# Performance work log

Hardware: AMD Instinct MI355X
Metric: run time of the kernel (lower is better)

## Reference

```python
import jax, jax.numpy as jnp
import numpy as np

EMBED_DIM = 1024
NUM_HEADS = 16
HEAD_DIM = EMBED_DIM // NUM_HEADS


def setup_inputs() -> dict:
    key = jax.random.key(0)
    ks = jax.random.split(key, 9)
    B, S, D = 2, 2048, EMBED_DIM
    scale = 1.0 / np.sqrt(D)
    x = jax.random.normal(ks[0], (B, S, D), dtype=jnp.float32)
    wq = jax.random.normal(ks[1], (D, D), dtype=jnp.float32) * scale
    bq = jax.random.normal(ks[2], (D,), dtype=jnp.float32) * 0.02
    wk = jax.random.normal(ks[3], (D, D), dtype=jnp.float32) * scale
    bk = jax.random.normal(ks[4], (D,), dtype=jnp.float32) * 0.02
    wv = jax.random.normal(ks[5], (D, D), dtype=jnp.float32) * scale
    bv = jax.random.normal(ks[6], (D,), dtype=jnp.float32) * 0.02
    wo = jax.random.normal(ks[7], (D, D), dtype=jnp.float32) * scale
    bo = jax.random.normal(ks[8], (D,), dtype=jnp.float32) * 0.02
    return {"x": x, "wq": wq, "bq": bq, "wk": wk, "bk": bk,
            "wv": wv, "bv": bv, "wo": wo, "bo": bo}


def reference(x, wq, bq, wk, bk, wv, bv, wo, bo):
    B, S, D = x.shape
    H, Hd = NUM_HEADS, HEAD_DIM
    # separate QKV linears (weights stored [in, out] so x @ w)
    q = (x @ wq + bq).reshape(B, S, H, Hd).transpose(0, 2, 1, 3)  # [B,H,S,Hd]
    k = (x @ wk + bk).reshape(B, S, H, Hd).transpose(0, 2, 1, 3)
    v = (x @ wv + bv).reshape(B, S, H, Hd).transpose(0, 2, 1, 3)
    scores = jnp.einsum('bhqd,bhkd->bhqk', q, k) / jnp.sqrt(jnp.float32(Hd))
    attn = jax.nn.softmax(scores, axis=-1)
    context = jnp.einsum('bhqk,bhkd->bhqd', attn, v)
    context = context.transpose(0, 2, 1, 3).reshape(B, S, D)
    return context @ wo + bo
```

## Files before the change

### kernel.cpp

```cpp
#include <hip/hip_runtime.h>
#include <cstdint>
#include <cstddef>


typedef float floatx4 __attribute__((ext_vector_type(4)));
typedef __bf16 bf16x8 __attribute__((ext_vector_type(8)));
union ABFrag { bf16x8 v; uint4 q; unsigned short u[8]; unsigned int w[4]; };

__device__ __forceinline__ unsigned short f2bf(float f) {
    unsigned int u = __builtin_bit_cast(unsigned int, f);
    return (unsigned short)((u + 0x7FFFu + ((u >> 16) & 1u)) >> 16);
}

__device__ __forceinline__ unsigned int pkbf(float lo, float hi) {
    unsigned int a = __builtin_bit_cast(unsigned int, hi) + 0x8000u;
    unsigned int b = __builtin_bit_cast(unsigned int, lo) + 0x8000u;
    return __builtin_amdgcn_perm(a, b, 0x07060302u);
}

#if __has_builtin(__builtin_amdgcn_exp2f)
#define EXP2F(x) __builtin_amdgcn_exp2f(x)
#else
#define EXP2F(x) exp2f(x)
#endif

__device__ __forceinline__ void glds16(const void* g, void* l) {
    __builtin_amdgcn_global_load_lds(
        (const __attribute__((address_space(1))) unsigned int*)(uintptr_t)g,
        (__attribute__((address_space(3))) unsigned int*)(unsigned int)(uintptr_t)l,
        16, 0, 0);
}

__global__ void convert_x_kernel(const float* __restrict__ x,
                                 unsigned short* __restrict__ xb) {
    int i = (blockIdx.x * 256 + threadIdx.x) * 8;
    float4 a = *(const float4*)(x + i);
    float4 b = *(const float4*)(x + i + 4);
    union { unsigned short u[8]; uint4 q; } o;
    o.u[0] = f2bf(a.x); o.u[1] = f2bf(a.y); o.u[2] = f2bf(a.z); o.u[3] = f2bf(a.w);
    o.u[4] = f2bf(b.x); o.u[5] = f2bf(b.y); o.u[6] = f2bf(b.z); o.u[7] = f2bf(b.w);
    *(uint4*)(xb + i) = o.q;
}

__global__ void convert_wT_kernel(const float* __restrict__ w0, const float* __restrict__ w1,
                                  const float* __restrict__ w2, const float* __restrict__ w3,
                                  unsigned short* __restrict__ wT) {
    __shared__ unsigned short t[32][40];
    const float* w = (blockIdx.z == 0) ? w0 : (blockIdx.z == 1) ? w1
                   : (blockIdx.z == 2) ? w2 : w3;
    unsigned short* dst = wT + (size_t)blockIdx.z * 1024 * 1024;
    const int k0 = blockIdx.x * 32, n0 = blockIdx.y * 32;
    const int tid = threadIdx.x;
    {
        int ry = tid >> 3, cx = (tid & 7) * 4;
        float4 v = *(const float4*)(w + (size_t)(k0 + ry) * 1024 + n0 + cx);
        t[cx + 0][ry] = f2bf(v.x); t[cx + 1][ry] = f2bf(v.y);
        t[cx + 2][ry] = f2bf(v.z); t[cx + 3][ry] = f2bf(v.w);
    }
    __syncthreads();
    int n = tid >> 3, kc = (tid & 7) * 4;
    *(uint2*)(dst + (size_t)(n0 + n) * 1024 + k0 + kc) = *(const uint2*)&t[n][kc];
}

template<int KIND>
__launch_bounds__(256, 2)
__global__ void gemm_kernel(const unsigned short* __restrict__ A,
                            const unsigned short* __restrict__ wT,
                            const float* __restrict__ bias0,
                            const float* __restrict__ bias1,
                            const float* __restrict__ bias2,
                            void* __restrict__ out0,
                            void* __restrict__ out1,
                            void* __restrict__ out2)
{
    __shared__ unsigned short a_s[128 * 32];
    __shared__ unsigned short b_s[128 * 32];

    const int tid  = threadIdx.x;
    const int wid  = tid >> 6;
    const int lane = tid & 63;
    const int quad = lane >> 4;
    const int l15  = lane & 15;
    const int wm   = (wid >> 1) * 64;
    const int wn   = (wid & 1) * 64;
    const int m0   = blockIdx.y * 128;
    const int n0   = blockIdx.x * 128;

    const unsigned short* Bt = (KIND == 0) ? wT + (size_t)blockIdx.z * (1024 * 1024) : wT;
    const float* bias = (KIND == 0)
        ? (blockIdx.z == 0 ? bias0 : blockIdx.z == 1 ? bias1 : bias2) : bias0;

    const int sr = lane >> 2;
    const int sc = (lane & 3) * 8;
    const unsigned short* gA = A  + (size_t)(m0 + wid * 32 + sr) * 1024 + sc;
    const unsigned short* gB = Bt + (size_t)(n0 + wid * 32 + sr) * 1024 + sc;
    unsigned short* lA = a_s + wid * 1024;
    unsigned short* lB = b_s + wid * 1024;

    floatx4 acc[4][4];
    #pragma unroll
    for (int i = 0; i < 4; i++)
        #pragma unroll
        for (int j = 0; j < 4; j++)
            acc[i][j] = floatx4{0.f, 0.f, 0.f, 0.f};

    for (int k0 = 0; k0 < 1024; k0 += 32) {
        __syncthreads();
        glds16(gA + k0,             lA);
        glds16(gA + k0 + 16 * 1024, lA + 512);
        glds16(gB + k0,             lB);
        glds16(gB + k0 + 16 * 1024, lB + 512);
        __syncthreads();

        ABFrag af[4], bf4[4];
        #pragma unroll
        for (int i = 0; i < 4; i++)
            af[i].q = *(const uint4*)(a_s + (wm + i * 16 + l15) * 32 + quad * 8);
        #pragma unroll
        for (int j = 0; j < 4; j++)
            bf4[j].q = *(const uint4*)(b_s + (wn + j * 16 + l15) * 32 + quad * 8);
        #pragma unroll
        for (int i = 0; i < 4; i++)
            #pragma unroll
            for (int j = 0; j < 4; j++)
                acc[i][j] = __builtin_amdgcn_mfma_f32_16x16x32_bf16(
                    af[i].v, bf4[j].v, acc[i][j], 0, 0, 0);
    }

    if constexpr (KIND == 1) {
        float* out = (float*)out0;
        #pragma unroll
        for (int j = 0; j < 4; j++) {
            int gn = n0 + wn + j * 16 + l15;
            float bval = bias[gn];
            #pragma unroll
            for (int i = 0; i < 4; i++)
                #pragma unroll
                for (int r = 0; r < 4; r++) {
                    int gm = m0 + wm + i * 16 + quad * 4 + r;
                    out[(size_t)gm * 1024 + gn] = acc[i][j][r] + bval;
                }
        }
    } else {
        if (blockIdx.z == 0) {
            const float SCQ = 0.125f * 1.44269504088896f;
            unsigned short* out = (unsigned short*)out0;
            #pragma unroll
            for (int j = 0; j < 4; j++) {
                int gn = n0 + wn + j * 16 + l15;
                float bval = bias[gn];
                int h = gn >> 6, d = gn & 63;
                #pragma unroll
                for (int i = 0; i < 4; i++)
                    #pragma unroll
                    for (int r = 0; r < 4; r++) {
                        int gm = m0 + wm + i * 16 + quad * 4 + r;
                        int b = gm >> 11, s = gm & 2047;
                        out[(((size_t)(b * 16 + h) * 2048 + s) << 6) + d] =
                            f2bf((acc[i][j][r] + bval) * SCQ);
                    }
            }
        } else if (blockIdx.z == 1) {
            unsigned short* out = (unsigned short*)out1;
            #pragma unroll
            for (int j = 0; j < 4; j++) {
                int gn = n0 + wn + j * 16 + l15;
                float bval = bias[gn];
                int h = gn >> 6, d = gn & 63;
                int dg = d >> 3, dl = d & 7;
                #pragma unroll
                for (int i = 0; i < 4; i++)
                    #pragma unroll
                    for (int r = 0; r < 4; r++) {
                        int gm = m0 + wm + i * 16 + quad * 4 + r;
                        int b = gm >> 11, s = gm & 2047;
                        int dphys = ((dg ^ (s & 7)) << 3) | dl;
                        out[(((size_t)(b * 16 + h) * 2048 + s) << 6) + dphys] =
                            f2bf(acc[i][j][r] + bval);
                    }
            }
        } else {
            __shared__ unsigned short t_s[128][136];
            #pragma unroll
            for (int j = 0; j < 4; j++) {
                int nl = wn + j * 16 + l15;
                float bval = bias[n0 + nl];
                #pragma unroll
                for (int i = 0; i < 4; i++)
                    #pragma unroll
                    for (int r = 0; r < 4; r++)
                        t_s[nl][wm + i * 16 + quad * 4 + r] = f2bf(acc[i][j][r] + bval);
            }
            __syncthreads();
            unsigned short* out = (unsigned short*)out2;
            const int n  = tid >> 1, half = tid & 1;
            const int bh = (m0 >> 11) * 16 + ((n0 + n) >> 6);
            const int d  = (n0 + n) & 63;
            const int chunk = ((m0 & 2047) >> 6) + half;
            const int dmask = d & 7;
            unsigned short* dstb = out + ((size_t)(bh * 32 + chunk) * 64 + d) * 64;
            const unsigned short* src = &t_s[n][half * 64];
            #pragma unroll
            for (int gp = 0; gp < 8; gp++) {
                int u1 = 32 * (gp >> 2) + 4 * (gp & 3);
                uint2 lo = *(const uint2*)(src + u1);
                uint2 hi = *(const uint2*)(src + u1 + 16);
                unsigned short* dq = dstb + ((gp ^ dmask) << 3);
                *(uint2*)dq       = lo;
                *(uint2*)(dq + 4) = hi;
            }
        }
    }
}

__launch_bounds__(256, 2)
__global__ void attn_kernel(const unsigned short* __restrict__ Q,
                            const unsigned short* __restrict__ K,
                            const unsigned short* __restrict__ Vt,
                            unsigned short* __restrict__ ctx)
{
    __shared__ unsigned short smem[2][2][4096];

    const int tid  = threadIdx.x;
    const int wid  = tid >> 6;
    const int lane = tid & 63;
    const int quad = lane >> 4;
    const int l15  = lane & 15;
    const int xr   = l15 & 7;

    const int bh = blockIdx.y;
    const unsigned short* Qh = Q + (size_t)bh * (2048 * 64);
    const char* Kc = (const char*)(K  + (size_t)bh * (2048 * 64));
    const char* Vc = (const char*)(Vt + (size_t)bh * (2048 * 64));
    const int q0 = blockIdx.x * 128 + wid * 32;

    ABFrag qf[2][2];
    #pragma unroll
    for (int jq = 0; jq < 2; jq++)
        #pragma unroll
        for (int s = 0; s < 2; s++)
            qf[jq][s].q = *(const uint4*)(Qh + (size_t)(q0 + jq * 16 + l15) * 64
                                          + s * 32 + quad * 8);

    int kcol[2], vcol[2];
    kcol[0] = ((quad    ) ^ xr) << 3;
    kcol[1] = ((quad + 4) ^ xr) << 3;
    vcol[0] = ((quad    ) ^ xr) << 3;
    vcol[1] = ((quad + 4) ^ xr) << 3;

    floatx4 acc[4][2];
    #pragma unroll
    for (int i = 0; i < 4; i++)
        #pragma unroll
        for (int jq = 0; jq < 2; jq++)
            acc[i][jq] = floatx4{0.f, 0.f, 0.f, 0.f};
    float lrun[2] = {0.f, 0.f};

    auto stage = [&](int c, int b) {
        const char* gk = Kc + (size_t)c * 8192 + wid * 2048 + lane * 16;
        char* lk = (char*)&smem[b][0][0] + wid * 2048;
        glds16(gk,        lk);
        glds16(gk + 1024, lk + 1024);
        const char* gv = Vc + (size_t)c * 8192 + wid * 2048 + lane * 16;
        char* lv = (char*)&smem[b][1][0] + wid * 2048;
        glds16(gv,        lv);
        glds16(gv + 1024, lv + 1024);
    };

    stage(0, 0);

    for (int c = 0; c < 32; ++c) {
        const int b = c & 1;
        __syncthreads();
        if (c + 1 < 32) stage(c + 1, b ^ 1);

        const unsigned short* ks = &smem[b][0][0];
        const unsigned short* vs = &smem[b][1][0];

        floatx4 st[4][2];
        #pragma unroll
        for (int kt = 0; kt < 4; kt++) {
            ABFrag k0, k1;
            const unsigned short* kr = ks + (kt * 16 + l15) * 64;
            k0.q = *(const uint4*)(kr + kcol[0]);
            k1.q = *(const uint4*)(kr + kcol[1]);
            #pragma unroll
            for (int jq = 0; jq < 2; jq++) {
                floatx4 t = floatx4{0.f, 0.f, 0.f, 0.f};
                t = __builtin_amdgcn_mfma_f32_16x16x32_bf16(k0.v, qf[jq][0].v, t, 0, 0, 0);
                t = __builtin_amdgcn_mfma_f32_16x16x32_bf16(k1.v, qf[jq][1].v, t, 0, 0, 0);
                st[kt][jq] = t;
            }
        }

        unsigned int pk[4][2][2];
        #pragma unroll
        for (int jq = 0; jq < 2; jq++) {
            float ls = 0.f;
            #pragma unroll
            for (int kt = 0; kt < 4; kt++) {
                #pragma unroll
                for (int t2 = 0; t2 < 2; t2++) {
                    float p0 = EXP2F(st[kt][jq][2 * t2 + 0]);
                    float p1 = EXP2F(st[kt][jq][2 * t2 + 1]);
                    ls += p0 + p1;
                    pk[kt][jq][t2] = pkbf(p0, p1);
                }
            }
            lrun[jq] += ls;
        }

        #pragma unroll
        for (int s2 = 0; s2 < 2; s2++) {
            ABFrag pf[2];
            #pragma unroll
            for (int jq = 0; jq < 2; jq++) {
                pf[jq].w[0] = pk[2 * s2 + 0][jq][0];
                pf[jq].w[1] = pk[2 * s2 + 0][jq][1];
                pf[jq].w[2] = pk[2 * s2 + 1][jq][0];
                pf[jq].w[3] = pk[2 * s2 + 1][jq][1];
            }
            #pragma unroll
            for (int i = 0; i < 4; i++) {
                ABFrag vf;
                vf.q = *(const uint4*)(vs + (i * 16 + l15) * 64 + vcol[s2]);
                #pragma unroll
                for (int jq = 0; jq < 2; jq++)
                    acc[i][jq] = __builtin_amdgcn_mfma_f32_16x16x32_bf16(
                        vf.v, pf[jq].v, acc[i][jq], 0, 0, 0);
            }
        }
    }

    const int b_ = bh >> 4, h = bh & 15;
    #pragma unroll
    for (int jq = 0; jq < 2; jq++) {
        float s = lrun[jq];
        s += __shfl_xor(s, 16, 64);
        s += __shfl_xor(s, 32, 64);
        float inv = 1.0f / s;
        int q = q0 + jq * 16 + l15;
        size_t base = (size_t)(b_ * 2048 + q) * 1024 + h * 64;
        #pragma unroll
        for (int i = 0; i < 4; i++) {
            float v0 = acc[i][jq][0] * inv, v1 = acc[i][jq][1] * inv;
            float v2 = acc[i][jq][2] * inv, v3 = acc[i][jq][3] * inv;
            uint2 w2 = make_uint2(pkbf(v0, v1), pkbf(v2, v3));
            *(uint2*)(ctx + base + i * 16 + quad * 4) = w2;
        }
    }
}

extern "C" void kernel_launch(void* const* d_in, const int* in_sizes, int n_in,
                              void* d_out, int out_size, void* d_ws, size_t ws_size,
                              hipStream_t stream)
{
    const float* x  = (const float*)d_in[0];
    const float* wq = (const float*)d_in[1];
    const float* bq = (const float*)d_in[2];
    const float* wk = (const float*)d_in[3];
    const float* bk = (const float*)d_in[4];
    const float* wv = (const float*)d_in[5];
    const float* bv = (const float*)d_in[6];
    const float* wo = (const float*)d_in[7];
    const float* bo = (const float*)d_in[8];

    const size_t NE = (size_t)4096 * 1024;
    unsigned short* xb  = (unsigned short*)d_ws;
    unsigned short* wT  = xb  + NE;
    unsigned short* qb  = wT  + NE;
    unsigned short* kb  = qb  + NE;
    unsigned short* vtb = kb  + NE;
    unsigned short* ctx = vtb + NE;

    hipLaunchKernelGGL(convert_x_kernel, dim3(2048), dim3(256), 0, stream, x, xb);
    hipLaunchKernelGGL(convert_wT_kernel, dim3(32, 32, 4), dim3(256), 0, stream,
                       wq, wk, wv, wo, wT);
    hipLaunchKernelGGL((gemm_kernel<0>), dim3(8, 32, 3), dim3(256), 0, stream,
                       xb, wT, bq, bk, bv, (void*)qb, (void*)kb, (void*)vtb);
    hipLaunchKernelGGL(attn_kernel, dim3(16, 32), dim3(256), 0, stream, qb, kb, vtb, ctx);
    hipLaunchKernelGGL((gemm_kernel<1>), dim3(8, 32), dim3(256), 0, stream,
                       ctx, wT + 3 * NE / 4, bo, nullptr, nullptr, d_out, nullptr, nullptr);
}
```

Measured before the change: 197.3 us.

## Swap MFMA operands for vectorized epilogues and halve attention tile per wave

The QK projection GEMM swaps its MFMA operand order so each lane holds four consecutive output columns, which lets the Q/K and output-projection epilogues write packed uint2 or float4 stores instead of scalar ones. V is split into its own GEMM instantiation that writes the transposed, swizzled layout directly from registers, removing the LDS transpose buffer and its extra barrier. The attention kernel drops to 16 queries per wave (64 per block, twice as many blocks) to cut register use and raise occupancy, at the cost of reloading K/V tiles for twice as many blocks. Launch bounds are raised to allow more resident blocks, and the QKV projection now takes two launches instead of one.

```diff
diff --git a/kernel.cpp b/kernel.cpp
--- a/kernel.cpp
+++ b/kernel.cpp
@@ -63,15 +63,13 @@
 }
 
 template<int KIND>
-__launch_bounds__(256, 2)
+__launch_bounds__(256, 3)
 __global__ void gemm_kernel(const unsigned short* __restrict__ A,
-                            const unsigned short* __restrict__ wT,
+                            const unsigned short* __restrict__ Bt,
                             const float* __restrict__ bias0,
                             const float* __restrict__ bias1,
-                            const float* __restrict__ bias2,
                             void* __restrict__ out0,
-                            void* __restrict__ out1,
-                            void* __restrict__ out2)
+                            void* __restrict__ out1)
 {
     __shared__ unsigned short a_s[128 * 32];
     __shared__ unsigned short b_s[128 * 32];
@@ -86,14 +84,14 @@
     const int m0   = blockIdx.y * 128;
     const int n0   = blockIdx.x * 128;
 
-    const unsigned short* Bt = (KIND == 0) ? wT + (size_t)blockIdx.z * (1024 * 1024) : wT;
-    const float* bias = (KIND == 0)
-        ? (blockIdx.z == 0 ? bias0 : blockIdx.z == 1 ? bias1 : bias2) : bias0;
+    const int z = (KIND == 0) ? blockIdx.z : 0;
+    const unsigned short* Bw = Bt + (size_t)z * (1024 * 1024);
+    const float* bias = (KIND == 0 && z == 1) ? bias1 : bias0;
 
     const int sr = lane >> 2;
     const int sc = (lane & 3) * 8;
     const unsigned short* gA = A  + (size_t)(m0 + wid * 32 + sr) * 1024 + sc;
-    const unsigned short* gB = Bt + (size_t)(n0 + wid * 32 + sr) * 1024 + sc;
+    const unsigned short* gB = Bw + (size_t)(n0 + wid * 32 + sr) * 1024 + sc;
     unsigned short* lA = a_s + wid * 1024;
     unsigned short* lB = b_s + wid * 1024;
 
@@ -122,98 +120,80 @@
         #pragma unroll
         for (int i = 0; i < 4; i++)
             #pragma unroll
-            for (int j = 0; j < 4; j++)
-                acc[i][j] = __builtin_amdgcn_mfma_f32_16x16x32_bf16(
-                    af[i].v, bf4[j].v, acc[i][j], 0, 0, 0);
-    }
-
-    if constexpr (KIND == 1) {
+            for (int j = 0; j < 4; j++) {
+                if (KIND == 1)
+                    acc[i][j] = __builtin_amdgcn_mfma_f32_16x16x32_bf16(
+                        af[i].v, bf4[j].v, acc[i][j], 0, 0, 0);
+                else
+                    acc[i][j] = __builtin_amdgcn_mfma_f32_16x16x32_bf16(
+                        bf4[i].v, af[j].v, acc[i][j], 0, 0, 0);
+            }
+    }
+
+    if constexpr (KIND == 2) {
         float* out = (float*)out0;
+        #pragma unroll
+        for (int i = 0; i < 4; i++) {
+            int gnb = n0 + wn + i * 16 + quad * 4;
+            float4 bv4 = *(const float4*)(bias + gnb);
+            #pragma unroll
+            for (int j = 0; j < 4; j++) {
+                int gm = m0 + wm + j * 16 + l15;
+                float4 o = make_float4(acc[i][j][0] + bv4.x, acc[i][j][1] + bv4.y,
+                                       acc[i][j][2] + bv4.z, acc[i][j][3] + bv4.w);
+                *(float4*)(out + (size_t)gm * 1024 + gnb) = o;
+            }
+        }
+    } else if constexpr (KIND == 0) {
+        const float SCQ = 0.125f * 1.44269504088896f;
+        unsigned short* out = (unsigned short*)(z == 0 ? out0 : out1);
+        #pragma unroll
+        for (int i = 0; i < 4; i++) {
+            int gnb = n0 + wn + i * 16 + quad * 4;
+            float4 bv4 = *(const float4*)(bias + gnb);
+            int h = gnb >> 6, db = gnb & 63;
+            #pragma unroll
+            for (int j = 0; j < 4; j++) {
+                int s = m0 + wm + j * 16 + l15;
+                int b = s >> 11, srow = s & 2047;
+                size_t rowb = ((size_t)(b * 16 + h) * 2048 + srow) * 64;
+                float v0 = acc[i][j][0] + bv4.x, v1 = acc[i][j][1] + bv4.y;
+                float v2 = acc[i][j][2] + bv4.z, v3 = acc[i][j][3] + bv4.w;
+                size_t addr;
+                if (z == 0) {
+                    v0 *= SCQ; v1 *= SCQ; v2 *= SCQ; v3 *= SCQ;
+                    addr = rowb + db;
+                } else {
+                    addr = rowb + (size_t)((((db >> 3) ^ (srow & 7)) << 3) + (db & 7));
+                }
+                uint2 w2 = make_uint2(pkbf(v0, v1), pkbf(v2, v3));
+                *(uint2*)(out + addr) = w2;
+            }
+        }
+    } else {
+        unsigned short* out = (unsigned short*)out0;
         #pragma unroll
         for (int j = 0; j < 4; j++) {
             int gn = n0 + wn + j * 16 + l15;
             float bval = bias[gn];
-            #pragma unroll
-            for (int i = 0; i < 4; i++)
-                #pragma unroll
-                for (int r = 0; r < 4; r++) {
-                    int gm = m0 + wm + i * 16 + quad * 4 + r;
-                    out[(size_t)gm * 1024 + gn] = acc[i][j][r] + bval;
-                }
-        }
-    } else {
-        if (blockIdx.z == 0) {
-            const float SCQ = 0.125f * 1.44269504088896f;
-            unsigned short* out = (unsigned short*)out0;
-            #pragma unroll
-            for (int j = 0; j < 4; j++) {
-                int gn = n0 + wn + j * 16 + l15;
-                float bval = bias[gn];
-                int h = gn >> 6, d = gn & 63;
-                #pragma unroll
-                for (int i = 0; i < 4; i++)
-                    #pragma unroll
-                    for (int r = 0; r < 4; r++) {
-                        int gm = m0 + wm + i * 16 + quad * 4 + r;
-                        int b = gm >> 11, s = gm & 2047;
-                        out[(((size_t)(b * 16 + h) * 2048 + s) << 6) + d] =
-                            f2bf((acc[i][j][r] + bval) * SCQ);
-                    }
-            }
-        } else if (blockIdx.z == 1) {
-            unsigned short* out = (unsigned short*)out1;
-            #pragma unroll
-            for (int j = 0; j < 4; j++) {
-                int gn = n0 + wn + j * 16 + l15;
-                float bval = bias[gn];
-                int h = gn >> 6, d = gn & 63;
-                int dg = d >> 3, dl = d & 7;
-                #pragma unroll
-                for (int i = 0; i < 4; i++)
-                    #pragma unroll
-                    for (int r = 0; r < 4; r++) {
-                        int gm = m0 + wm + i * 16 + quad * 4 + r;
-                        int b = gm >> 11, s = gm & 2047;
-                        int dphys = ((dg ^ (s & 7)) << 3) | dl;
-                        out[(((size_t)(b * 16 + h) * 2048 + s) << 6) + dphys] =
-                            f2bf(acc[i][j][r] + bval);
-                    }
-            }
-        } else {
-            __shared__ unsigned short t_s[128][136];
-            #pragma unroll
-            for (int j = 0; j < 4; j++) {
-                int nl = wn + j * 16 + l15;
-                float bval = bias[n0 + nl];
-                #pragma unroll
-                for (int i = 0; i < 4; i++)
-                    #pragma unroll
-                    for (int r = 0; r < 4; r++)
-                        t_s[nl][wm + i * 16 + quad * 4 + r] = f2bf(acc[i][j][r] + bval);
-            }
-            __syncthreads();
-            unsigned short* out = (unsigned short*)out2;
-            const int n  = tid >> 1, half = tid & 1;
-            const int bh = (m0 >> 11) * 16 + ((n0 + n) >> 6);
-            const int d  = (n0 + n) & 63;
-            const int chunk = ((m0 & 2047) >> 6) + half;
-            const int dmask = d & 7;
-            unsigned short* dstb = out + ((size_t)(bh * 32 + chunk) * 64 + d) * 64;
-            const unsigned short* src = &t_s[n][half * 64];
-            #pragma unroll
-            for (int gp = 0; gp < 8; gp++) {
-                int u1 = 32 * (gp >> 2) + 4 * (gp & 3);
-                uint2 lo = *(const uint2*)(src + u1);
-                uint2 hi = *(const uint2*)(src + u1 + 16);
-                unsigned short* dq = dstb + ((gp ^ dmask) << 3);
-                *(uint2*)dq       = lo;
-                *(uint2*)(dq + 4) = hi;
-            }
-        }
-    }
-}
-
-__launch_bounds__(256, 2)
+            int h = gn >> 6, d = gn & 63, dx = d & 7;
+            #pragma unroll
+            for (int i = 0; i < 4; i++) {
+                int gmb = m0 + wm + i * 16 + quad * 4;
+                int b = gmb >> 11, cg = (gmb & 2047) >> 6;
+                int gp = (((i >> 1) * 4 + quad) ^ dx);
+                size_t addr = ((size_t)((b * 16 + h) * 32 + cg) * 64 + d) * 64
+                              + (gp << 3) + (i & 1) * 4;
+                float v0 = acc[i][j][0] + bval, v1 = acc[i][j][1] + bval;
+                float v2 = acc[i][j][2] + bval, v3 = acc[i][j][3] + bval;
+                uint2 w2 = make_uint2(pkbf(v0, v1), pkbf(v2, v3));
+                *(uint2*)(out + addr) = w2;
+            }
+        }
+    }
+}
+
+__launch_bounds__(256, 4)
 __global__ void attn_kernel(const unsigned short* __restrict__ Q,
                             const unsigned short* __restrict__ K,
                             const unsigned short* __restrict__ Vt,
@@ -232,15 +212,12 @@
     const unsigned short* Qh = Q + (size_t)bh * (2048 * 64);
     const char* Kc = (const char*)(K  + (size_t)bh * (2048 * 64));
     const char* Vc = (const char*)(Vt + (size_t)bh * (2048 * 64));
-    const int q0 = blockIdx.x * 128 + wid * 32;
-
-    ABFrag qf[2][2];
+    const int q0 = blockIdx.x * 64 + wid * 16;
+
+    ABFrag qf[2];
     #pragma unroll
-    for (int jq = 0; jq < 2; jq++)
-        #pragma unroll
-        for (int s = 0; s < 2; s++)
-            qf[jq][s].q = *(const uint4*)(Qh + (size_t)(q0 + jq * 16 + l15) * 64
-                                          + s * 32 + quad * 8);
+    for (int s = 0; s < 2; s++)
+        qf[s].q = *(const uint4*)(Qh + (size_t)(q0 + l15) * 64 + s * 32 + quad * 8);
 
     int kcol[2], vcol[2];
     kcol[0] = ((quad    ) ^ xr) << 3;
@@ -248,13 +225,10 @@
     vcol[0] = ((quad    ) ^ xr) << 3;
     vcol[1] = ((quad + 4) ^ xr) << 3;
 
-    floatx4 acc[4][2];
+    floatx4 acc[4];
     #pragma unroll
-    for (int i = 0; i < 4; i++)
-        #pragma unroll
-        for (int jq = 0; jq < 2; jq++)
-            acc[i][jq] = floatx4{0.f, 0.f, 0.f, 0.f};
-    float lrun[2] = {0.f, 0.f};
+    for (int i = 0; i < 4; i++) acc[i] = floatx4{0.f, 0.f, 0.f, 0.f};
+    float lrun = 0.f;
 
     auto stage = [&](int c, int b) {
         const char* gk = Kc + (size_t)c * 8192 + wid * 2048 + lane * 16;
@@ -277,77 +251,63 @@
         const unsigned short* ks = &smem[b][0][0];
         const unsigned short* vs = &smem[b][1][0];
 
-        floatx4 st[4][2];
+        floatx4 st[4];
         #pragma unroll
         for (int kt = 0; kt < 4; kt++) {
             ABFrag k0, k1;
             const unsigned short* kr = ks + (kt * 16 + l15) * 64;
             k0.q = *(const uint4*)(kr + kcol[0]);
             k1.q = *(const uint4*)(kr + kcol[1]);
-            #pragma unroll
-            for (int jq = 0; jq < 2; jq++) {
-                floatx4 t = floatx4{0.f, 0.f, 0.f, 0.f};
-                t = __builtin_amdgcn_mfma_f32_16x16x32_bf16(k0.v, qf[jq][0].v, t, 0, 0, 0);
-                t = __builtin_amdgcn_mfma_f32_16x16x32_bf16(k1.v, qf[jq][1].v, t, 0, 0, 0);
-                st[kt][jq] = t;
-            }
-        }
-
-        unsigned int pk[4][2][2];
-        #pragma unroll
-        for (int jq = 0; jq < 2; jq++) {
-            float ls = 0.f;
-            #pragma unroll
-            for (int kt = 0; kt < 4; kt++) {
-                #pragma unroll
-                for (int t2 = 0; t2 < 2; t2++) {
-                    float p0 = EXP2F(st[kt][jq][2 * t2 + 0]);
-                    float p1 = EXP2F(st[kt][jq][2 * t2 + 1]);
-                    ls += p0 + p1;
-                    pk[kt][jq][t2] = pkbf(p0, p1);
-                }
-            }
-            lrun[jq] += ls;
-        }
+            floatx4 t = floatx4{0.f, 0.f, 0.f, 0.f};
+            t = __builtin_amdgcn_mfma_f32_16x16x32_bf16(k0.v, qf[0].v, t, 0, 0, 0);
+            t = __builtin_amdgcn_mfma_f32_16x16x32_bf16(k1.v, qf[1].v, t, 0, 0, 0);
+            st[kt] = t;
+        }
+
+        unsigned int pk[4][2];
+        float ls = 0.f;
+        #pragma unroll
+        for (int kt = 0; kt < 4; kt++) {
+            #pragma unroll
+            for (int t2 = 0; t2 < 2; t2++) {
+                float p0 = EXP2F(st[kt][2 * t2 + 0]);
+                float p1 = EXP2F(st[kt][2 * t2 + 1]);
+                ls += p0 + p1;
+                pk[kt][t2] = pkbf(p0, p1);
+            }
+        }
+        lrun += ls;
 
         #pragma unroll
         for (int s2 = 0; s2 < 2; s2++) {
-            ABFrag pf[2];
-            #pragma unroll
-            for (int jq = 0; jq < 2; jq++) {
-                pf[jq].w[0] = pk[2 * s2 + 0][jq][0];
-                pf[jq].w[1] = pk[2 * s2 + 0][jq][1];
-                pf[jq].w[2] = pk[2 * s2 + 1][jq][0];
-                pf[jq].w[3] = pk[2 * s2 + 1][jq][1];
-            }
+            ABFrag pf;
+            pf.w[0] = pk[2 * s2 + 0][0];
+            pf.w[1] = pk[2 * s2 + 0][1];
+            pf.w[2] = pk[2 * s2 + 1][0];
+            pf.w[3] = pk[2 * s2 + 1][1];
             #pragma unroll
             for (int i = 0; i < 4; i++) {
                 ABFrag vf;
                 vf.q = *(const uint4*)(vs + (i * 16 + l15) * 64 + vcol[s2]);
-                #pragma unroll
-                for (int jq = 0; jq < 2; jq++)
-                    acc[i][jq] = __builtin_amdgcn_mfma_f32_16x16x32_bf16(
-                        vf.v, pf[jq].v, acc[i][jq], 0, 0, 0);
+                acc[i] = __builtin_amdgcn_mfma_f32_16x16x32_bf16(
+                    vf.v, pf.v, acc[i], 0, 0, 0);
             }
         }
     }
 
     const int b_ = bh >> 4, h = bh & 15;
+    float s = lrun;
+    s += __shfl_xor(s, 16, 64);
+    s += __shfl_xor(s, 32, 64);
+    float inv = 1.0f / s;
+    int q = q0 + l15;
+    size_t base = (size_t)(b_ * 2048 + q) * 1024 + h * 64;
     #pragma unroll
-    for (int jq = 0; jq < 2; jq++) {
-        float s = lrun[jq];
-        s += __shfl_xor(s, 16, 64);
-        s += __shfl_xor(s, 32, 64);
-        float inv = 1.0f / s;
-        int q = q0 + jq * 16 + l15;
-        size_t base = (size_t)(b_ * 2048 + q) * 1024 + h * 64;
-        #pragma unroll
-        for (int i = 0; i < 4; i++) {
-            float v0 = acc[i][jq][0] * inv, v1 = acc[i][jq][1] * inv;
-            float v2 = acc[i][jq][2] * inv, v3 = acc[i][jq][3] * inv;
-            uint2 w2 = make_uint2(pkbf(v0, v1), pkbf(v2, v3));
-            *(uint2*)(ctx + base + i * 16 + quad * 4) = w2;
-        }
+    for (int i = 0; i < 4; i++) {
+        float v0 = acc[i][0] * inv, v1 = acc[i][1] * inv;
+        float v2 = acc[i][2] * inv, v3 = acc[i][3] * inv;
+        uint2 w2 = make_uint2(pkbf(v0, v1), pkbf(v2, v3));
+        *(uint2*)(ctx + base + i * 16 + quad * 4) = w2;
     }
 }
 
@@ -366,6 +326,7 @@
     const float* bo = (const float*)d_in[8];
 
     const size_t NE = (size_t)4096 * 1024;
+    const size_t PLANE = (size_t)1024 * 1024;
     unsigned short* xb  = (unsigned short*)d_ws;
     unsigned short* wT  = xb  + NE;
     unsigned short* qb  = wT  + NE;
@@ -376,9 +337,11 @@
     hipLaunchKernelGGL(convert_x_kernel, dim3(2048), dim3(256), 0, stream, x, xb);
     hipLaunchKernelGGL(convert_wT_kernel, dim3(32, 32, 4), dim3(256), 0, stream,
                        wq, wk, wv, wo, wT);
-    hipLaunchKernelGGL((gemm_kernel<0>), dim3(8, 32, 3), dim3(256), 0, stream,
-                       xb, wT, bq, bk, bv, (void*)qb, (void*)kb, (void*)vtb);
-    hipLaunchKernelGGL(attn_kernel, dim3(16, 32), dim3(256), 0, stream, qb, kb, vtb, ctx);
-    hipLaunchKernelGGL((gemm_kernel<1>), dim3(8, 32), dim3(256), 0, stream,
-                       ctx, wT + 3 * NE / 4, bo, nullptr, nullptr, d_out, nullptr, nullptr);
-}
+    hipLaunchKernelGGL((gemm_kernel<0>), dim3(8, 32, 2), dim3(256), 0, stream,
+                       xb, wT, bq, bk, (void*)qb, (void*)kb);
+    hipLaunchKernelGGL((gemm_kernel<1>), dim3(8, 32, 1), dim3(256), 0, stream,
+                       xb, wT + 2 * PLANE, bv, nullptr, (void*)vtb, nullptr);
+    hipLaunchKernelGGL(attn_kernel, dim3(32, 32), dim3(256), 0, stream, qb, kb, vtb, ctx);
+    hipLaunchKernelGGL((gemm_kernel<2>), dim3(8, 32, 1), dim3(256), 0, stream,
+                       ctx, wT + 3 * PLANE, bo, nullptr, d_out, nullptr);
+}
```

Result: slower. 222.7 us (+12.9%).
